# Kernel optimization log

Measured on AMD Instinct MI355X. Metric: run time of the kernel, lower is better.

Reference implementation:

```python
import jax, jax.numpy as jnp
import numpy as np

E_QUBITS = 8  # embedding dim == number of qubits


def _iqp_amplitudes(x):
    """Statevector amplitudes of qml.IQPEmbedding(x) applied to |0..0>.

    x: [..., E] real. Returns [..., 2^E] complex64.
    Circuit: H on all wires, RZ(x_i) on wire i, MultiRZ(x_i*x_j) on all pairs i<j.
    For basis state z with signs s_i = (-1)^{z_i}:
      amp(z) = 2^{-E/2} * exp(i * phi(z)),
      phi(z) = -1/2 * sum_i x_i s_i - 1/2 * sum_{i<j} x_i x_j s_i s_j
             = -L/2 - (L^2 - ||x||^2)/4,  with L = sum_i x_i s_i.
    """
    E = x.shape[-1]
    z = jnp.arange(2 ** E)
    bits = (z[:, None] >> jnp.arange(E)[None, :]) & 1          # [2^E, E]
    s = (1.0 - 2.0 * bits).astype(x.dtype)                      # (-1)^{z_i}
    L = x @ s.T                                                 # [..., 2^E]
    sq = jnp.sum(x * x, axis=-1, keepdims=True)                 # ||x||^2
    phase = -0.5 * L - 0.25 * (L * L - sq)
    return jnp.exp(1j * phase) * (2.0 ** (-E / 2.0))            # complex64


def setup_inputs() -> dict:
    key = jax.random.key(0)
    kq, kk, kv = jax.random.split(key, 3)
    B, S, E = 16, 1024, E_QUBITS
    return {
        "Q": jax.random.normal(kq, (B, S, E), dtype=jnp.float32),
        "K": jax.random.normal(kk, (B, S, E), dtype=jnp.float32),
        "V": jax.random.normal(kv, (B, S, E), dtype=jnp.float32),
    }


def reference(Q, K, V):
    # Pure-state amplitudes for every token (IQP embedding). [B,S,2^E] complex
    aq = _iqp_amplitudes(Q)
    ak = _iqp_amplitudes(K)
    # Fidelity of pure states: |<psi_q|psi_k>|^2, batched Gram matrix.
    ip = jnp.einsum("bid,bjd->bij", jnp.conj(aq), ak)          # [B,S,S] complex
    fid = jnp.real(ip * jnp.conj(ip))                           # [B,S,S] float32
    attn = 2.0 * fid - 1.0
    return jnp.einsum("bij,bje->bie", attn, V)                  # [B,S,E]
```

## Files before the change

### kernel.cpp

```cpp
#include <hip/hip_runtime.h>
#include <hip/hip_bf16.h>
#include <stdint.h>

#define NB 16
#define S_LEN 1024
#define E_Q 8

typedef float v4f __attribute__((ext_vector_type(4)));
typedef short v8s __attribute__((ext_vector_type(8)));
typedef int   v4i __attribute__((ext_vector_type(4)));

__global__ __launch_bounds__(256) void build_tables(
    const float* __restrict__ Q, const float* __restrict__ K,
    int8_t* __restrict__ Aq, int8_t* __restrict__ Kt,
    float* __restrict__ out)
{
    const int which = blockIdx.y;
    const float* X = which ? K : Q;

    if (which == 0 && blockIdx.x < 128) {
        float4 z; z.x = z.y = z.z = z.w = 0.f;
        ((float4*)out)[blockIdx.x * 256 + threadIdx.x] = z;
    }

    const int tok = blockIdx.x * 16 + (threadIdx.x >> 4);
    const int hi  = threadIdx.x & 15;
    const int zb  = hi * 16;

    const float* x = X + tok * E_Q;
    float xv[E_Q]; float sq = 0.f;
#pragma unroll
    for (int i = 0; i < E_Q; ++i) { xv[i] = x[i]; sq += xv[i] * xv[i]; }
    const float qsq = 0.25f * sq;

    float L = xv[0] + xv[1] + xv[2] + xv[3];
#pragma unroll
    for (int i = 4; i < 8; ++i) L += ((hi >> (i - 4)) & 1) ? -xv[i] : xv[i];

    __align__(16) int8_t cb[16];
    __align__(16) int8_t sb[16];

    {
        const float phi = fmaf(-0.25f, L * L, fmaf(-0.5f, L, qsq));
        float s, c; __sincosf(phi, &s, &c);
        cb[0] = (int8_t)__float2int_rn(127.f * c);
        sb[0] = (int8_t)__float2int_rn(127.f * s);
    }
#pragma unroll
    for (int n = 1; n < 16; ++n) {
        const int g  = n ^ (n >> 1);
        const int gp = (n - 1) ^ ((n - 1) >> 1);
        const int t  = __builtin_ctz(g ^ gp);
        const float twox = 2.0f * xv[t];
        L = ((g >> t) & 1) ? (L - twox) : (L + twox);
        const float phi = fmaf(-0.25f, L * L, fmaf(-0.5f, L, qsq));
        float s, c; __sincosf(phi, &s, &c);
        cb[g] = (int8_t)__float2int_rn(127.f * c);
        sb[g] = (int8_t)__float2int_rn(127.f * s);
    }

    if (which == 0) {
        int8_t* dst = Aq + (size_t)tok * 512;
        *(uint4*)(dst + zb)       = *(const uint4*)cb;
        *(uint4*)(dst + 256 + zb) = *(const uint4*)sb;
    } else {
        __align__(16) int8_t nb[16];
#pragma unroll
        for (int i = 0; i < 16; ++i) nb[i] = (int8_t)(-cb[i]);
        int8_t* dst = Kt + (size_t)tok * 768;
        *(uint4*)(dst + zb)       = *(const uint4*)cb;
        *(uint4*)(dst + 256 + zb) = *(const uint4*)sb;
        *(uint4*)(dst + 512 + zb) = *(const uint4*)nb;
    }
}

__global__ __launch_bounds__(256, 2) void qk_pv(
    const int8_t* __restrict__ Aq, const int8_t* __restrict__ Kt,
    const float* __restrict__ V, float* __restrict__ out)
{
    __shared__ __align__(16) char smem[49152];
    int8_t* lA  = (int8_t*)smem;
    int8_t* lK0 = (int8_t*)(smem + 16384);
    int8_t* lK1 = (int8_t*)(smem + 32768);
    uint16_t* lattn = (uint16_t*)smem;
    uint16_t* lVt   = (uint16_t*)(smem + 34816);

    const int jblk = blockIdx.x, iblk = blockIdx.y, b = blockIdx.z;
    const int tid  = threadIdx.x;
    const int lane = tid & 63, wv = tid >> 6;
    const int wKj = wv >> 1, wQi = wv & 1;
    const int r15 = lane & 15, qq = lane >> 4;

    const int qsw   = (tid & 7) ^ ((tid >> 3) & 7);
    const int baseA = (tid >> 3) * 512 + qsw * 16;
    const int baseK = (tid >> 3) * 768 + qsw * 16;
    const int lbase = wv * 1024;

    const int8_t* gA = Aq + (size_t)(b * S_LEN + iblk * 128) * 512;
    const int8_t* gK = Kt + (size_t)(b * S_LEN + jblk * 128) * 768;

    v4i accRe[4][4], accIm[4][4];
#pragma unroll
    for (int nj = 0; nj < 4; ++nj)
#pragma unroll
        for (int mi = 0; mi < 4; ++mi) {
            accRe[nj][mi] = (v4i)0;
            accIm[nj][mi] = (v4i)0;
        }

    for (int c = 0; c < 4; ++c) {
        __syncthreads();
        const int cbyte = c * 128;
#pragma unroll
        for (int p = 0; p < 4; ++p) {
            const int lo = p * 4096 + lbase;
            __builtin_amdgcn_global_load_lds(
                (const __attribute__((address_space(1))) void*)(gA + cbyte + baseA + p * 16384),
                (__attribute__((address_space(3))) void*)(lA + lo), 16, 0, 0);
            __builtin_amdgcn_global_load_lds(
                (const __attribute__((address_space(1))) void*)(gK + cbyte + baseK + p * 24576),
                (__attribute__((address_space(3))) void*)(lK0 + lo), 16, 0, 0);
            __builtin_amdgcn_global_load_lds(
                (const __attribute__((address_space(1))) void*)(gK + 256 + cbyte + baseK + p * 24576),
                (__attribute__((address_space(3))) void*)(lK1 + lo), 16, 0, 0);
        }
        __syncthreads();

#pragma unroll
        for (int w = 0; w < 2; ++w) {
            v4i qF[4];
#pragma unroll
            for (int mi = 0; mi < 4; ++mi) {
                const int row = wQi * 64 + mi * 16 + r15;
                qF[mi] = *(const v4i*)&lA[row * 128 + (((w << 2) | qq) ^ (row & 7)) * 16];
            }
#pragma unroll
            for (int nj = 0; nj < 4; ++nj) {
                const int rk  = wKj * 64 + nj * 16 + r15;
                const int off = rk * 128 + (((w << 2) | qq) ^ (rk & 7)) * 16;
                const v4i k0 = *(const v4i*)&lK0[off];
                const v4i k1 = *(const v4i*)&lK1[off];
#pragma unroll
                for (int mi = 0; mi < 4; ++mi) {
                    accRe[nj][mi] = __builtin_amdgcn_mfma_i32_16x16x64_i8(k0, qF[mi], accRe[nj][mi], 0, 0, 0);
                    accIm[nj][mi] = __builtin_amdgcn_mfma_i32_16x16x64_i8(k1, qF[mi], accIm[nj][mi], 0, 0, 0);
                }
            }
        }
    }

    __syncthreads();

    const float4 vreg = ((const float4*)(V + ((size_t)b * S_LEN + jblk * 128) * E_Q))[tid];

    const float sc2 = 3.0517578125e-05f / 260144641.0f;
#pragma unroll
    for (int nj = 0; nj < 4; ++nj) {
#pragma unroll
        for (int mi = 0; mi < 4; ++mi) {
            uint64_t pk = 0;
#pragma unroll
            for (int rg = 0; rg < 4; ++rg) {
                const float rf  = (float)accRe[nj][mi][rg];
                const float imf = (float)accIm[nj][mi][rg];
                const float a   = fmaf(rf * rf + imf * imf, sc2, -1.0f);
                __hip_bfloat16 ab = __float2bfloat16(a);
                pk |= (uint64_t)(*(const uint16_t*)&ab) << (16 * rg);
            }
            const int i  = wQi * 64 + mi * 16 + r15;
            const int j0 = wKj * 64 + nj * 16 + qq * 4;
            *(uint64_t*)&lattn[i * 136 + j0] = pk;
        }
    }
    {
        const int j = tid >> 1, eh = (tid & 1) * 4;
        const float vv[4] = {vreg.x, vreg.y, vreg.z, vreg.w};
#pragma unroll
        for (int c2 = 0; c2 < 4; ++c2) {
            __hip_bfloat16 vb = __float2bfloat16(vv[c2]);
            lVt[(eh + c2) * 136 + j] = *(const uint16_t*)&vb;
        }
    }
    __syncthreads();

    v8s bfr[4];
#pragma unroll
    for (int ks3 = 0; ks3 < 4; ++ks3)
        bfr[ks3] = *(const v8s*)&lVt[r15 * 136 + ks3 * 32 + qq * 8];

    float* outb = out + (((size_t)b << 10) + iblk * 128) * E_Q;
#pragma unroll
    for (int mt = 0; mt < 2; ++mt) {
        const int rowbase = (wv * 2 + mt) * 16;
        v4f accO = (v4f)0.f;
#pragma unroll
        for (int ks3 = 0; ks3 < 4; ++ks3) {
            const v8s af = *(const v8s*)&lattn[(rowbase + r15) * 136 + ks3 * 32 + qq * 8];
            accO = __builtin_amdgcn_mfma_f32_16x16x32_bf16(af, bfr[ks3], accO, 0, 0, 0);
        }
        if (r15 < E_Q) {
            const int i0 = rowbase + qq * 4;
#pragma unroll
            for (int rg = 0; rg < 4; ++rg)
                atomicAdd(&outb[(i0 + rg) * E_Q + r15], accO[rg]);
        }
    }
}

extern "C" void kernel_launch(void* const* d_in, const int* in_sizes, int n_in,
                              void* d_out, int out_size, void* d_ws, size_t ws_size,
                              hipStream_t stream) {
    const float* Q = (const float*)d_in[0];
    const float* K = (const float*)d_in[1];
    const float* V = (const float*)d_in[2];
    float* out = (float*)d_out;

    int8_t* Aq = (int8_t*)d_ws;
    int8_t* Kt = (int8_t*)((char*)d_ws + (size_t)8 * 1024 * 1024);

    build_tables<<<dim3(NB * S_LEN / 16, 2), 256, 0, stream>>>(Q, K, Aq, Kt, out);
    qk_pv<<<dim3(S_LEN / 128, S_LEN / 128, NB), 256, 0, stream>>>(Aq, Kt, V, out);
}
```

Baseline: 87.14 us.

## Register-prefetch next K/Q chunk while computing current chunk in qk_pv

Replaces the direct global-to-LDS loads with register staging: the next chunk's A/K tiles are loaded into registers right after the current chunk is written to LDS. Those loads can then overlap with the MFMA work on the current chunk instead of stalling at the barrier. In exchange it uses 12 more vector registers per thread, which with launch bounds of 2 blocks per CU may cause spills or lower occupancy. It also adds explicit LDS store instructions.

```diff
diff --git a/kernel.cpp b/kernel.cpp
--- a/kernel.cpp
+++ b/kernel.cpp
@@ -94,10 +94,18 @@
     const int qsw   = (tid & 7) ^ ((tid >> 3) & 7);
     const int baseA = (tid >> 3) * 512 + qsw * 16;
     const int baseK = (tid >> 3) * 768 + qsw * 16;
-    const int lbase = wv * 1024;
+    const int tid16 = tid * 16;
 
     const int8_t* gA = Aq + (size_t)(b * S_LEN + iblk * 128) * 512;
     const int8_t* gK = Kt + (size_t)(b * S_LEN + jblk * 128) * 768;
+
+    v4i rA[4], rK0[4], rK1[4];
+#pragma unroll
+    for (int p = 0; p < 4; ++p) {
+        rA[p]  = *(const v4i*)(gA + baseA + p * 16384);
+        rK0[p] = *(const v4i*)(gK + baseK + p * 24576);
+        rK1[p] = *(const v4i*)(gK + 256 + baseK + p * 24576);
+    }
 
     v4i accRe[4][4], accIm[4][4];
 #pragma unroll
@@ -108,21 +116,23 @@
             accIm[nj][mi] = (v4i)0;
         }
 
+#pragma unroll 1
     for (int c = 0; c < 4; ++c) {
         __syncthreads();
-        const int cbyte = c * 128;
 #pragma unroll
         for (int p = 0; p < 4; ++p) {
-            const int lo = p * 4096 + lbase;
-            __builtin_amdgcn_global_load_lds(
-                (const __attribute__((address_space(1))) void*)(gA + cbyte + baseA + p * 16384),
-                (__attribute__((address_space(3))) void*)(lA + lo), 16, 0, 0);
-            __builtin_amdgcn_global_load_lds(
-                (const __attribute__((address_space(1))) void*)(gK + cbyte + baseK + p * 24576),
-                (__attribute__((address_space(3))) void*)(lK0 + lo), 16, 0, 0);
-            __builtin_amdgcn_global_load_lds(
-                (const __attribute__((address_space(1))) void*)(gK + 256 + cbyte + baseK + p * 24576),
-                (__attribute__((address_space(3))) void*)(lK1 + lo), 16, 0, 0);
+            *(v4i*)(lA  + p * 4096 + tid16) = rA[p];
+            *(v4i*)(lK0 + p * 4096 + tid16) = rK0[p];
+            *(v4i*)(lK1 + p * 4096 + tid16) = rK1[p];
+        }
+        if (c < 3) {
+            const int cb = (c + 1) * 128;
+#pragma unroll
+            for (int p = 0; p < 4; ++p) {
+                rA[p]  = *(const v4i*)(gA + cb + baseA + p * 16384);
+                rK0[p] = *(const v4i*)(gK + cb + baseK + p * 24576);
+                rK1[p] = *(const v4i*)(gK + 256 + cb + baseK + p * 24576);
+            }
         }
         __syncthreads();
 
```

New measurement: 89.59 us. 2.8% more time.
